# Optimization experiments

Measured on AMD Instinct MI355X. Metric: run time of the kernel, lower is better.

Reference implementation:

```python
import jax, jax.numpy as jnp
import numpy as np

V, D, L, H, HD, S = 50257, 768, 8, 6, 128, 2048
BS = 128          # flex-attention BLOCK_SIZE
EOS = 50256       # document separator token
EPS = 1.1920929e-07  # torch F.rms_norm default eps (f32 machine eps)
ATTN_SCALE = 0.12


def rms(x):
    return x * jax.lax.rsqrt(jnp.mean(jnp.square(x), axis=-1, keepdims=True) + EPS)


def rope_tables(seq_len, hd):
    # modded-nanogpt rotary: hd//4 geometric freqs + hd//4 zero freqs, applied to half-split dims
    freqs = (1.0 / 1024.0) ** jnp.linspace(0.0, 1.0, hd // 4)
    freqs = jnp.concatenate([freqs, jnp.zeros(hd // 4, dtype=jnp.float32)])
    theta = jnp.arange(seq_len, dtype=jnp.float32)[:, None] * freqs[None, :]  # [S, hd//2]
    return jnp.cos(theta), jnp.sin(theta)


def rope(x, cos, sin):  # x: [B,S,H,hd]
    x1, x2 = jnp.split(x, 2, axis=-1)
    c = cos[None, :, None, :]
    s = sin[None, :, None, :]
    return jnp.concatenate([x1 * c + x2 * s, -x1 * s + x2 * c], axis=-1)


def build_token_mask(input_seq, w):
    # Reproduces BlockMask.from_kv_blocks semantics: per query-row keep the w-1 most
    # recent FULL blocks and min(n_partial, max(w - n_full, 1)) most recent PARTIAL
    # blocks; mask_mod (document-causal) applies inside partial blocks only.
    NB = S // BS
    docs = jnp.cumsum((input_seq == EOS).astype(jnp.int32))
    bi = jnp.arange(NB)
    dr = docs.reshape(NB, BS)
    dl, dh = dr[:, 0], dr[:, -1]
    m_any = (bi[:, None] >= bi[None, :]) & (dl[:, None] <= dh[None, :]) & (dh[:, None] >= dl[None, :])
    m_all = (bi[:, None] > bi[None, :]) & (dl[:, None] == dh[None, :]) & (dh[:, None] == dl[None, :])
    part = m_any & ~m_all
    nf = m_all.sum(-1)

    def keep_most_recent(m, kcount):  # keep kcount True entries with largest kv index
        r = jnp.cumsum(m[:, ::-1].astype(jnp.int32), axis=-1)[:, ::-1]
        return m & (r <= kcount[:, None])

    kf = keep_most_recent(m_all, jnp.minimum(nf, w - 1))
    kp = keep_most_recent(part, jnp.minimum(part.sum(-1), jnp.maximum(w - nf, 1)))
    tf = jnp.repeat(jnp.repeat(kf, BS, 0), BS, 1)   # [S,S]
    tp = jnp.repeat(jnp.repeat(kp, BS, 0), BS, 1)
    q = jnp.arange(S)
    tok = (q[:, None] >= q[None, :]) & (docs[:, None] == docs[None, :])
    return tf | (tp & tok)


def _forward(input_seq, sliding_window_num_blocks, target_seq, embed, ve_embeds,
             qkv_w, attn_proj_w, mlp_fc_w, mlp_proj_w, scalars):
    cos, sin = rope_tables(S, HD)
    long_m = build_token_mask(input_seq, sliding_window_num_blocks)
    short_m = build_token_mask(input_seq, sliding_window_num_blocks // 2)
    cycle = [long_m, short_m, short_m, short_m]
    masks = (cycle * ((L + 3) // 4))[:L - 1] + [long_m]

    ve_tok = ve_embeds[:, input_seq, :]  # [3,S,D]
    ve = [ve_tok[0], ve_tok[1], ve_tok[2]] + [None] * (L - 6) + [ve_tok[0], ve_tok[1], ve_tok[2]]

    skip_w = scalars[:L]
    lambdas = scalars[L:3 * L].reshape(L, 2)
    sa_lambdas = scalars[3 * L:5 * L].reshape(L, 2)

    stride = max(1, L // 4)
    skip_map = {}
    for m in range(3):
        i = L - 3 + m
        j = i - stride * (m + 1)
        if 0 <= j < i < L:
            skip_map[i] = j

    x = x0 = rms(embed[input_seq])[None]  # [1,S,D]
    skips = []
    for i in range(L):
        if i in skip_map:
            x = x + skip_w[skip_map[i]] * skips[skip_map[i]]
        lam, sal = lambdas[i], sa_lambdas[i]
        # Block: residual mix with x0, attn, mlp (modded-nanogpt style)
        x = lam[0] * x + lam[1] * x0
        xa = rms(x)
        qkv = (xa @ qkv_w[i].T).reshape(1, S, 3 * H, HD)
        q, k, v = jnp.split(qkv, 3, axis=2)
        q = rope(rms(q), cos, sin)
        k = rope(rms(k), cos, sin)
        if ve[i] is not None:
            v = sal[0] * v + sal[1] * ve[i].reshape(1, S, H, HD)
        else:
            v = sal[0] * v
        scores = jnp.einsum('bqhd,bkhd->bhqk', q, k) * ATTN_SCALE
        scores = jnp.where(masks[i][None, None], scores, -jnp.inf)
        y = jnp.einsum('bhqk,bkhd->bqhd', jax.nn.softmax(scores, axis=-1), v)
        x = x + y.reshape(1, S, H * HD) @ attn_proj_w[i].T
        h = jnp.square(jax.nn.relu(rms(x) @ mlp_fc_w[i].T))
        x = x + h @ mlp_proj_w[i].T
        skips.append(x)

    x = rms(x)
    logits = (x[0].astype(jnp.bfloat16) @ embed.T.astype(jnp.bfloat16)).astype(jnp.float32)
    cap = 15.0 * logits * jax.lax.rsqrt(jnp.square(logits) + 225.0)  # softcap
    lsm = jax.nn.log_softmax(cap, axis=-1)
    return -jnp.mean(lsm[jnp.arange(S), target_seq])


def setup_inputs() -> dict:
    key = jax.random.key(0)
    ks = jax.random.split(key, 9)
    input_seq = jax.random.randint(ks[0], (S,), 0, V)
    input_seq = input_seq.at[jnp.arange(0, S, 512)].set(EOS)  # inject doc boundaries
    target_seq = jax.random.randint(ks[1], (S,), 0, V)
    embed = jax.random.normal(ks[2], (V, D), jnp.float32)
    ve_embeds = jax.random.normal(ks[3], (3, V, D), jnp.float32)
    sd = 1.0 / np.sqrt(D)
    qkv_w = jax.random.normal(ks[4], (L, 3 * H * HD, D), jnp.float32) * sd
    attn_proj_w = jax.random.normal(ks[5], (L, D, H * HD), jnp.float32) * (1.0 / np.sqrt(H * HD))
    mlp_fc_w = jax.random.normal(ks[6], (L, 4 * D, D), jnp.float32) * sd
    mlp_proj_w = jax.random.normal(ks[7], (L, D, 4 * D), jnp.float32) * (1.0 / np.sqrt(4 * D))
    scalars = jnp.concatenate([
        jnp.ones(L), jnp.tile(jnp.array([1.0, 0.0]), L), jnp.tile(jnp.array([0.5, 0.5]), L)
    ]).astype(jnp.float32) + 0.02 * jax.random.normal(ks[8], (5 * L,), jnp.float32)
    return {"input_seq": input_seq, "sliding_window_num_blocks": 8, "target_seq": target_seq,
            "embed": embed, "ve_embeds": ve_embeds, "qkv_w": qkv_w, "attn_proj_w": attn_proj_w,
            "mlp_fc_w": mlp_fc_w, "mlp_proj_w": mlp_proj_w, "scalars": scalars}


def reference(input_seq, sliding_window_num_blocks, target_seq, embed, ve_embeds,
              qkv_w, attn_proj_w, mlp_fc_w, mlp_proj_w, scalars):
    return _forward(input_seq, sliding_window_num_blocks, target_seq, embed, ve_embeds,
                    qkv_w, attn_proj_w, mlp_fc_w, mlp_proj_w, scalars)
```

## Files before the change

### kernel.cpp

```cpp
#include <hip/hip_runtime.h>
#include <hip/hip_bf16.h>
#include <math.h>

#define NSEQ 2048
#define NDIM 768
#define NLAY 8
#define NHEAD 6
#define NHD 128
#define NVOC 50257
#define NBLK 16
#define BLKSZ 128
#define EOS_TOK 50256
#define EPSF 1.1920929e-07f
#define ASCALE 0.12f
#define NVT 393

using bf16x8 = __attribute__((ext_vector_type(8))) __bf16;
using bf16x4 = __attribute__((ext_vector_type(4))) __bf16;
using f32x4  = __attribute__((ext_vector_type(4))) float;

__device__ __forceinline__ __bf16 tobf(float x) {
  __hip_bfloat16 h = __float2bfloat16(x);
  return *reinterpret_cast<__bf16*>(&h);
}

__global__ __launch_bounds__(256) void cvt_bf16_kernel(const float* __restrict__ in, __bf16* __restrict__ out,
                                                       long n) {
  long i = ((long)blockIdx.x * blockDim.x + threadIdx.x) * 4;
  long stride = (long)gridDim.x * blockDim.x * 4;
  for (; i < n; i += stride) {
    float4 v = *(const float4*)(in + i);
    bf16x4 o;
    o[0] = tobf(v.x); o[1] = tobf(v.y); o[2] = tobf(v.z); o[3] = tobf(v.w);
    *(bf16x4*)(out + i) = o;
  }
}

__global__ __launch_bounds__(1024) void prep_kernel(const int* __restrict__ seq, const int* __restrict__ wptr,
                                                    int* __restrict__ docs, int* __restrict__ catL,
                                                    int* __restrict__ catS) {
  __shared__ int f[NSEQ];
  __shared__ int g[NSEQ];
  int tid = threadIdx.x;
  for (int i = tid; i < NSEQ; i += 1024) f[i] = (seq[i] == EOS_TOK) ? 1 : 0;
  __syncthreads();
  int* a = f; int* b = g;
  for (int off = 1; off < NSEQ; off <<= 1) {
    for (int i = tid; i < NSEQ; i += 1024) {
      int v = a[i];
      if (i >= off) v += a[i - off];
      b[i] = v;
    }
    __syncthreads();
    int* t = a; a = b; b = t;
  }
  for (int i = tid; i < NSEQ; i += 1024) docs[i] = a[i];
  __syncthreads();
  if (tid == 0) {
    int dl[NBLK], dh[NBLK];
    for (int bi = 0; bi < NBLK; ++bi) { dl[bi] = a[bi * BLKSZ]; dh[bi] = a[bi * BLKSZ + BLKSZ - 1]; }
    int W = *wptr;
    for (int pass = 0; pass < 2; ++pass) {
      int w = (pass == 0) ? W : (W / 2);
      int* cat = (pass == 0) ? catL : catS;
      for (int i = 0; i < NBLK; ++i) {
        int allr[NBLK], partr[NBLK];
        int nf = 0, np = 0;
        for (int j = 0; j < NBLK; ++j) {
          int any_ = (i >= j) && (dl[i] <= dh[j]) && (dh[i] >= dl[j]);
          int all_ = (i > j) && (dl[i] == dh[j]) && (dh[i] == dl[j]);
          allr[j] = all_; partr[j] = any_ && !all_;
          nf += all_; np += partr[j];
        }
        int kcf = min(nf, w - 1);
        int kcp = min(np, max(w - nf, 1));
        int cf = 0, cp = 0;
        for (int j = NBLK - 1; j >= 0; --j) {
          int cv = 0;
          if (allr[j]) { cf++; if (cf <= kcf) cv = 2; }
          if (partr[j]) { cp++; if (cp <= kcp) cv = 1; }
          cat[i * NBLK + j] = cv;
        }
      }
    }
  }
}

__global__ __launch_bounds__(256) void embed_rms_kernel(const int* __restrict__ seq, const float* __restrict__ embed,
                                                        float* __restrict__ x, float* __restrict__ x0) {
  int s = blockIdx.x;
  int tid = threadIdx.x;
  const float* row = embed + (size_t)seq[s] * NDIM;
  float v0 = row[tid], v1 = row[tid + 256], v2 = row[tid + 512];
  float ss = v0 * v0 + v1 * v1 + v2 * v2;
  __shared__ float red[256];
  red[tid] = ss; __syncthreads();
  for (int o = 128; o > 0; o >>= 1) { if (tid < o) red[tid] += red[tid + o]; __syncthreads(); }
  float sc = rsqrtf(red[0] / (float)NDIM + EPSF);
  size_t base = (size_t)s * NDIM;
  float o0 = v0 * sc, o1 = v1 * sc, o2 = v2 * sc;
  x[base + tid] = o0; x[base + tid + 256] = o1; x[base + tid + 512] = o2;
  x0[base + tid] = o0; x0[base + tid + 256] = o1; x0[base + tid + 512] = o2;
}

__global__ __launch_bounds__(256) void rmsbf_kernel(const float* __restrict__ x, __bf16* __restrict__ xb) {
  int s = blockIdx.x;
  int tid = threadIdx.x;
  size_t base = (size_t)s * NDIM;
  float v0 = x[base + tid], v1 = x[base + tid + 256], v2 = x[base + tid + 512];
  float ss = v0 * v0 + v1 * v1 + v2 * v2;
  __shared__ float red[256];
  red[tid] = ss; __syncthreads();
  for (int o = 128; o > 0; o >>= 1) { if (tid < o) red[tid] += red[tid + o]; __syncthreads(); }
  float sc = rsqrtf(red[0] / (float)NDIM + EPSF);
  xb[base + tid] = tobf(v0 * sc); xb[base + tid + 256] = tobf(v1 * sc); xb[base + tid + 512] = tobf(v2 * sc);
}

__global__ __launch_bounds__(256) void mixrms_kernel(float* __restrict__ x, const float* __restrict__ x0,
                                                     const float* __restrict__ skip, const float* __restrict__ scal,
                                                     int li, int sj, __bf16* __restrict__ xb) {
  float lam0 = scal[NLAY + 2 * li], lam1 = scal[NLAY + 2 * li + 1];
  float sw = (sj >= 0) ? scal[sj] : 0.f;
  int s = blockIdx.x;
  int tid = threadIdx.x;
  size_t base = (size_t)s * NDIM;
  float xv[3], ov[3], nv[3];
  xv[0] = x[base + tid]; xv[1] = x[base + tid + 256]; xv[2] = x[base + tid + 512];
  ov[0] = x0[base + tid]; ov[1] = x0[base + tid + 256]; ov[2] = x0[base + tid + 512];
  if (skip) {
    nv[0] = lam0 * (xv[0] + sw * skip[base + tid])       + lam1 * ov[0];
    nv[1] = lam0 * (xv[1] + sw * skip[base + tid + 256]) + lam1 * ov[1];
    nv[2] = lam0 * (xv[2] + sw * skip[base + tid + 512]) + lam1 * ov[2];
  } else {
    nv[0] = lam0 * xv[0] + lam1 * ov[0];
    nv[1] = lam0 * xv[1] + lam1 * ov[1];
    nv[2] = lam0 * xv[2] + lam1 * ov[2];
  }
  x[base + tid] = nv[0]; x[base + tid + 256] = nv[1]; x[base + tid + 512] = nv[2];
  float ss = nv[0] * nv[0] + nv[1] * nv[1] + nv[2] * nv[2];
  __shared__ float red[256];
  red[tid] = ss; __syncthreads();
  for (int o = 128; o > 0; o >>= 1) { if (tid < o) red[tid] += red[tid + o]; __syncthreads(); }
  float sc = rsqrtf(red[0] / (float)NDIM + EPSF);
  xb[base + tid] = tobf(nv[0] * sc); xb[base + tid + 256] = tobf(nv[1] * sc); xb[base + tid + 512] = tobf(nv[2] * sc);
}

template <int MODE>
__global__ __launch_bounds__(256) void gemm_mfma(const __bf16* __restrict__ A, const __bf16* __restrict__ B,
                                                 float* __restrict__ Cf, __bf16* __restrict__ Cb,
                                                 int N, int K) {
  __shared__ __bf16 As[2][128 * 32];
  __shared__ __bf16 Bs[2][128 * 32];
  int bm = blockIdx.x * 128, bn = blockIdx.y * 128;
  int tid = threadIdx.x;
  int w = tid >> 6, l = tid & 63;
  int wm = (w >> 1) * 64, wn = (w & 1) * 64;
  int c = l & 15, g = l >> 4;

  auto stage = [&](int buf, int k0) {
#pragma unroll
    for (int i = 0; i < 2; ++i) {
      int L = (w * 2 + i) * 64 + l;
      int row = L >> 2, gc = L & 3;
      const __bf16* srcA = A + (size_t)(bm + row) * K + k0 + gc * 8;
      const __bf16* srcB = B + (size_t)(bn + row) * K + k0 + gc * 8;
      __builtin_amdgcn_global_load_lds(
          (const __attribute__((address_space(1))) void*)srcA,
          (__attribute__((address_space(3))) void*)&As[buf][(w * 2 + i) * 512], 16, 0, 0);
      __builtin_amdgcn_global_load_lds(
          (const __attribute__((address_space(1))) void*)srcB,
          (__attribute__((address_space(3))) void*)&Bs[buf][(w * 2 + i) * 512], 16, 0, 0);
    }
  };

  f32x4 acc[4][4] = {};
  stage(0, 0);
  __syncthreads();
  int nk = K >> 5;
  for (int kk = 0; kk < nk; ++kk) {
    int buf = kk & 1;
    if (kk + 1 < nk) stage(buf ^ 1, (kk + 1) * 32);
    bf16x8 af[4], bfr[4];
#pragma unroll
    for (int i = 0; i < 4; ++i) af[i] = *(const bf16x8*)&As[buf][(wm + i * 16 + c) * 32 + g * 8];
#pragma unroll
    for (int j = 0; j < 4; ++j) bfr[j] = *(const bf16x8*)&Bs[buf][(wn + j * 16 + c) * 32 + g * 8];
#pragma unroll
    for (int i = 0; i < 4; ++i)
#pragma unroll
      for (int j = 0; j < 4; ++j)
        acc[i][j] = __builtin_amdgcn_mfma_f32_16x16x32_bf16(af[i], bfr[j], acc[i][j], 0, 0, 0);
    __syncthreads();
  }
#pragma unroll
  for (int i = 0; i < 4; ++i)
#pragma unroll
    for (int j = 0; j < 4; ++j)
#pragma unroll
      for (int rr = 0; rr < 4; ++rr) {
        int row = bm + wm + i * 16 + g * 4 + rr;
        int col = bn + wn + j * 16 + c;
        size_t ci = (size_t)row * N + col;
        float z = acc[i][j][rr];
        if (MODE == 0) Cf[ci] = z;
        else if (MODE == 1) Cf[ci] += z;
        else { float r = fmaxf(z, 0.f); Cb[ci] = tobf(r * r); }
      }
}

template <int MODE>
__global__ __launch_bounds__(256) void gemm_mfma64(const __bf16* __restrict__ A, const __bf16* __restrict__ B,
                                                   float* __restrict__ Cf, __bf16* __restrict__ Cb,
                                                   int N, int K) {
  __shared__ __bf16 As[2][64 * 32];
  __shared__ __bf16 Bs[2][64 * 32];
  int bm = blockIdx.x * 64, bn = blockIdx.y * 64;
  int tid = threadIdx.x;
  int w = tid >> 6, l = tid & 63;
  int wm = (w >> 1) * 32, wn = (w & 1) * 32;
  int c = l & 15, g = l >> 4;

  auto stage = [&](int buf, int k0) {
    int L = w * 64 + l;
    int row = L >> 2, gc = L & 3;
    const __bf16* srcA = A + (size_t)(bm + row) * K + k0 + gc * 8;
    const __bf16* srcB = B + (size_t)(bn + row) * K + k0 + gc * 8;
    __builtin_amdgcn_global_load_lds(
        (const __attribute__((address_space(1))) void*)srcA,
        (__attribute__((address_space(3))) void*)&As[buf][w * 512], 16, 0, 0);
    __builtin_amdgcn_global_load_lds(
        (const __attribute__((address_space(1))) void*)srcB,
        (__attribute__((address_space(3))) void*)&Bs[buf][w * 512], 16, 0, 0);
  };

  f32x4 acc[2][2] = {};
  stage(0, 0);
  __syncthreads();
  int nk = K >> 5;
  for (int kk = 0; kk < nk; ++kk) {
    int buf = kk & 1;
    if (kk + 1 < nk) stage(buf ^ 1, (kk + 1) * 32);
    bf16x8 af[2], bfr[2];
#pragma unroll
    for (int i = 0; i < 2; ++i) af[i] = *(const bf16x8*)&As[buf][(wm + i * 16 + c) * 32 + g * 8];
#pragma unroll
    for (int j = 0; j < 2; ++j) bfr[j] = *(const bf16x8*)&Bs[buf][(wn + j * 16 + c) * 32 + g * 8];
#pragma unroll
    for (int i = 0; i < 2; ++i)
#pragma unroll
      for (int j = 0; j < 2; ++j)
        acc[i][j] = __builtin_amdgcn_mfma_f32_16x16x32_bf16(af[i], bfr[j], acc[i][j], 0, 0, 0);
    __syncthreads();
  }
#pragma unroll
  for (int i = 0; i < 2; ++i)
#pragma unroll
    for (int j = 0; j < 2; ++j)
#pragma unroll
      for (int rr = 0; rr < 4; ++rr) {
        int row = bm + wm + i * 16 + g * 4 + rr;
        int col = bn + wn + j * 16 + c;
        size_t ci = (size_t)row * N + col;
        float z = acc[i][j][rr];
        if (MODE == 0) Cf[ci] = z;
        else if (MODE == 1) Cf[ci] += z;
        else { float r = fmaxf(z, 0.f); Cb[ci] = tobf(r * r); }
      }
}

__global__ __launch_bounds__(256) void qkv_post_kernel(const float* __restrict__ qkv, const float* __restrict__ vemb,
                                                       const int* __restrict__ seq, const float* __restrict__ scal,
                                                       int li, int ve_idx,
                                                       __bf16* __restrict__ qo, __bf16* __restrict__ ko,
                                                       __bf16* __restrict__ vo) {
  int p = blockIdx.x * 4 + (threadIdx.x >> 6);
  int l = threadIdx.x & 63;
  int h = p >> 11;
  int s = p & (NSEQ - 1);
  float sal0 = scal[3 * NLAY + 2 * li], sal1 = scal[3 * NLAY + 2 * li + 1];
  float fr = (l < 32) ? powf(1.0f / 1024.0f, (float)l * (1.0f / 31.0f)) : 0.f;
  float th = (float)s * fr;
  float cth = cosf(th), sth = sinf(th);
  size_t rb = (size_t)s * (3 * NHEAD * NHD) + h * NHD;
  float q0 = qkv[rb + l],                 q1 = qkv[rb + l + 64];
  float k0 = qkv[rb + NHEAD * NHD + l],   k1 = qkv[rb + NHEAD * NHD + l + 64];
  float v0 = qkv[rb + 2 * NHEAD * NHD + l], v1 = qkv[rb + 2 * NHEAD * NHD + l + 64];
  float ssq = q0 * q0 + q1 * q1;
  float ssk = k0 * k0 + k1 * k1;
#pragma unroll
  for (int o = 1; o < 64; o <<= 1) {
    ssq += __shfl_xor(ssq, o, 64);
    ssk += __shfl_xor(ssk, o, 64);
  }
  float scq = rsqrtf(ssq / (float)NHD + EPSF);
  float sck = rsqrtf(ssk / (float)NHD + EPSF);
  float qn0 = q0 * scq, qn1 = q1 * scq;
  float kn0 = k0 * sck, kn1 = k1 * sck;
  float oq0 = qn0 * cth + qn1 * sth, oq1 = -qn0 * sth + qn1 * cth;
  float ok0 = kn0 * cth + kn1 * sth, ok1 = -kn0 * sth + kn1 * cth;
  float ov0 = sal0 * v0, ov1 = sal0 * v1;
  if (ve_idx >= 0) {
    const float* ver = vemb + ((size_t)ve_idx * NVOC + seq[s]) * NDIM + h * NHD;
    ov0 += sal1 * ver[l];
    ov1 += sal1 * ver[l + 64];
  }
  size_t oo = ((size_t)h * NSEQ + s) * NHD;
  qo[oo + l] = tobf(oq0); qo[oo + l + 64] = tobf(oq1);
  ko[oo + l] = tobf(ok0); ko[oo + l + 64] = tobf(ok1);
  vo[oo + l] = tobf(ov0); vo[oo + l + 64] = tobf(ov1);
}

__global__ __launch_bounds__(256) void vtrans_kernel(const __bf16* __restrict__ v, __bf16* __restrict__ vt) {
  int st = blockIdx.x * 64, dt = blockIdx.y * 64, h = blockIdx.z;
  __shared__ __bf16 t[64][65];
  int tid = threadIdx.x;
  for (int e = tid; e < 4096; e += 256) {
    int s = e >> 6, d = e & 63;
    t[s][d] = v[((size_t)h * NSEQ + st + s) * NHD + dt + d];
  }
  __syncthreads();
  for (int e = tid; e < 512; e += 256) {
    int d = e >> 3, s0 = (e & 7) * 8;
    bf16x8 ov;
#pragma unroll
    for (int i = 0; i < 8; ++i) ov[i] = t[s0 + i][d];
    *(bf16x8*)(vt + ((size_t)h * NHD + dt + d) * NSEQ + st + s0) = ov;
  }
}

__global__ __launch_bounds__(128) void attn_mfma_kernel(const __bf16* __restrict__ qb, const __bf16* __restrict__ kb,
                                                        const __bf16* __restrict__ vt, const int* __restrict__ cat,
                                                        const int* __restrict__ docs, __bf16* __restrict__ y) {
  int qb32 = (int)gridDim.x - 1 - (int)blockIdx.x;
  int h = blockIdx.y;
  int tid = threadIdx.x;
  int wq = tid >> 6;
  int l = tid & 63;
  int c = l & 15, g = l >> 4;
  int q0 = qb32 * 32 + wq * 16;
  int qB = qb32 >> 2;

  __shared__ __bf16 Ks[2][32 * 128];
  __shared__ __bf16 Vts[2][32 * 128];
  __shared__ __bf16 Ps[2][16 * 32];
  __shared__ int kvs[64];
  __shared__ int kvc[64];
  __shared__ int nact_s;

  if (tid == 0) {
    int n = 0;
    for (int kv = 0; kv <= qb32; ++kv) {
      int cc = cat[qB * NBLK + (kv >> 2)];
      if (cc) { kvs[n] = kv; kvc[n] = cc; ++n; }
    }
    nact_s = n;
  }

  bf16x8 qf[4];
#pragma unroll
  for (int ks = 0; ks < 4; ++ks)
    qf[ks] = *(const bf16x8*)(qb + ((size_t)h * NSEQ + q0 + c) * NHD + ks * 32 + g * 8);

  int qd[4];
#pragma unroll
  for (int rr = 0; rr < 4; ++rr) qd[rr] = docs[q0 + g * 4 + rr];

  float m[4], lden[4];
#pragma unroll
  for (int rr = 0; rr < 4; ++rr) { m[rr] = -INFINITY; lden[rr] = 0.f; }
  f32x4 oacc[8] = {};

  __syncthreads();
  int nact = nact_s;

  auto stage = [&](int kv, int bufi) {
#pragma unroll
    for (int i = 0; i < 4; ++i) {
      int L = (wq * 4 + i) * 64 + l;
      int krow = L >> 4, gl = L & 15;
      int gs = gl ^ (krow & 7);
      const __bf16* srcK = kb + ((size_t)h * NSEQ + kv * 32 + krow) * NHD + gs * 8;
      __builtin_amdgcn_global_load_lds(
          (const __attribute__((address_space(1))) void*)srcK,
          (__attribute__((address_space(3))) void*)&Ks[bufi][(wq * 4 + i) * 512], 16, 0, 0);
      int drow = L >> 2, gk = L & 3;
      const __bf16* srcV = vt + ((size_t)h * NHD + drow) * NSEQ + kv * 32 + gk * 8;
      __builtin_amdgcn_global_load_lds(
          (const __attribute__((address_space(1))) void*)srcV,
          (__attribute__((address_space(3))) void*)&Vts[bufi][(wq * 4 + i) * 512], 16, 0, 0);
    }
  };

  stage(kvs[0], 0);
  __syncthreads();

  for (int it = 0; it < nact; ++it) {
    int buf = it & 1;
    if (it + 1 < nact) stage(kvs[it + 1], buf ^ 1);
    int kv = kvs[it], cc = kvc[it];
    int k0 = kv * 32;

    f32x4 sacc[2] = {};
#pragma unroll
    for (int ks = 0; ks < 4; ++ks) {
#pragma unroll
      for (int j = 0; j < 2; ++j) {
        int row = j * 16 + c;
        int gi = (ks * 4 + g) ^ (row & 7);
        bf16x8 kf = *(const bf16x8*)&Ks[buf][row * 128 + gi * 8];
        sacc[j] = __builtin_amdgcn_mfma_f32_16x16x32_bf16(qf[ks], kf, sacc[j], 0, 0, 0);
      }
    }
    float sc[2][4];
    float bmax[4] = {-INFINITY, -INFINITY, -INFINITY, -INFINITY};
#pragma unroll
    for (int j = 0; j < 2; ++j) {
      int key = k0 + j * 16 + c;
      int kdj = docs[key];
#pragma unroll
      for (int rr = 0; rr < 4; ++rr) {
        int qrow = q0 + g * 4 + rr;
        bool ok = (cc == 2) || ((key <= qrow) && (kdj == qd[rr]));
        float z = ok ? sacc[j][rr] * ASCALE : -INFINITY;
        sc[j][rr] = z;
        bmax[rr] = fmaxf(bmax[rr], z);
      }
    }
#pragma unroll
    for (int rr = 0; rr < 4; ++rr) {
      bmax[rr] = fmaxf(bmax[rr], __shfl_xor(bmax[rr], 1, 64));
      bmax[rr] = fmaxf(bmax[rr], __shfl_xor(bmax[rr], 2, 64));
      bmax[rr] = fmaxf(bmax[rr], __shfl_xor(bmax[rr], 4, 64));
      bmax[rr] = fmaxf(bmax[rr], __shfl_xor(bmax[rr], 8, 64));
    }
    float corr[4], psum[4];
#pragma unroll
    for (int rr = 0; rr < 4; ++rr) {
      float mnew = fmaxf(m[rr], bmax[rr]);
      float msafe = (mnew == -INFINITY) ? 0.f : mnew;
      corr[rr] = __expf(m[rr] - msafe);
      float p0 = __expf(sc[0][rr] - msafe);
      float p1 = __expf(sc[1][rr] - msafe);
      sc[0][rr] = p0; sc[1][rr] = p1;
      psum[rr] = p0 + p1;
      m[rr] = mnew;
    }
#pragma unroll
    for (int rr = 0; rr < 4; ++rr) {
      psum[rr] += __shfl_xor(psum[rr], 1, 64);
      psum[rr] += __shfl_xor(psum[rr], 2, 64);
      psum[rr] += __shfl_xor(psum[rr], 4, 64);
      psum[rr] += __shfl_xor(psum[rr], 8, 64);
      lden[rr] = lden[rr] * corr[rr] + psum[rr];
    }
#pragma unroll
    for (int nt = 0; nt < 8; ++nt)
#pragma unroll
      for (int rr = 0; rr < 4; ++rr) oacc[nt][rr] *= corr[rr];
#pragma unroll
    for (int j = 0; j < 2; ++j)
#pragma unroll
      for (int rr = 0; rr < 4; ++rr)
        Ps[wq][(g * 4 + rr) * 32 + j * 16 + c] = tobf(sc[j][rr]);
    asm volatile("s_waitcnt lgkmcnt(0)" ::: "memory");
    bf16x8 pf = *(const bf16x8*)&Ps[wq][c * 32 + g * 8];
#pragma unroll
    for (int nt = 0; nt < 8; ++nt) {
      bf16x8 vf = *(const bf16x8*)&Vts[buf][(nt * 16 + c) * 32 + g * 8];
      oacc[nt] = __builtin_amdgcn_mfma_f32_16x16x32_bf16(pf, vf, oacc[nt], 0, 0, 0);
    }
    __syncthreads();
  }
  float inv[4];
#pragma unroll
  for (int rr = 0; rr < 4; ++rr) inv[rr] = (lden[rr] > 0.f) ? 1.f / lden[rr] : 0.f;
#pragma unroll
  for (int nt = 0; nt < 8; ++nt)
#pragma unroll
    for (int rr = 0; rr < 4; ++rr) {
      int qrow = q0 + g * 4 + rr;
      y[(size_t)qrow * NDIM + h * NHD + nt * 16 + c] = tobf(oacc[nt][rr] * inv[rr]);
    }
}

__global__ __launch_bounds__(256) void logits_gemm_kernel(const __bf16* __restrict__ xbf,
                                                          const __bf16* __restrict__ embed_bf,
                                                          const int* __restrict__ target,
                                                          float* __restrict__ part_m, float* __restrict__ part_l,
                                                          float* __restrict__ tcap) {
  __shared__ __bf16 As[2][128 * 32];
  __shared__ __bf16 Bs[2][128 * 32];
  __shared__ float rm2[2][128];
  __shared__ float rs2[2][128];
  int bm = blockIdx.x * 128;
  int vt = blockIdx.y;
  int bn = vt * 128;
  int tid = threadIdx.x;
  int w = tid >> 6, l = tid & 63;
  int wm = (w >> 1) * 64, wn = (w & 1) * 64;
  int c = l & 15, g = l >> 4;

  auto stage = [&](int buf, int k0) {
#pragma unroll
    for (int i = 0; i < 2; ++i) {
      int L = (w * 2 + i) * 64 + l;
      int row = L >> 2, gc = L & 3;
      int vrow = bn + row;
      if (vrow >= NVOC) vrow = NVOC - 1;
      const __bf16* srcA = xbf + (size_t)(bm + row) * NDIM + k0 + gc * 8;
      const __bf16* srcB = embed_bf + (size_t)vrow * NDIM + k0 + gc * 8;
      __builtin_amdgcn_global_load_lds(
          (const __attribute__((address_space(1))) void*)srcA,
          (__attribute__((address_space(3))) void*)&As[buf][(w * 2 + i) * 512], 16, 0, 0);
      __builtin_amdgcn_global_load_lds(
          (const __attribute__((address_space(1))) void*)srcB,
          (__attribute__((address_space(3))) void*)&Bs[buf][(w * 2 + i) * 512], 16, 0, 0);
    }
  };

  f32x4 acc[4][4] = {};
  stage(0, 0);
  __syncthreads();
  const int nk = NDIM / 32;
  for (int kk = 0; kk < nk; ++kk) {
    int buf = kk & 1;
    if (kk + 1 < nk) stage(buf ^ 1, (kk + 1) * 32);
    bf16x8 af[4], bfr[4];
#pragma unroll
    for (int i = 0; i < 4; ++i) af[i] = *(const bf16x8*)&As[buf][(wm + i * 16 + c) * 32 + g * 8];
#pragma unroll
    for (int j = 0; j < 4; ++j) bfr[j] = *(const bf16x8*)&Bs[buf][(wn + j * 16 + c) * 32 + g * 8];
#pragma unroll
    for (int i = 0; i < 4; ++i)
#pragma unroll
      for (int j = 0; j < 4; ++j)
        acc[i][j] = __builtin_amdgcn_mfma_f32_16x16x32_bf16(af[i], bfr[j], acc[i][j], 0, 0, 0);
    __syncthreads();
  }

#pragma unroll
  for (int i = 0; i < 4; ++i) {
#pragma unroll
    for (int rr = 0; rr < 4; ++rr) {
      int rowl = wm + i * 16 + g * 4 + rr;
      int tg = target[bm + rowl];
      float tmax = -INFINITY;
#pragma unroll
      for (int j = 0; j < 4; ++j) {
        int vv = bn + wn + j * 16 + c;
        bool okv = vv < NVOC;
        float z = acc[i][j][rr];
        float cp = okv ? 15.f * z * rsqrtf(z * z + 225.f) : -INFINITY;
        tmax = fmaxf(tmax, cp);
        if (okv && vv == tg) tcap[bm + rowl] = cp;
      }
      tmax = fmaxf(tmax, __shfl_xor(tmax, 1, 64));
      tmax = fmaxf(tmax, __shfl_xor(tmax, 2, 64));
      tmax = fmaxf(tmax, __shfl_xor(tmax, 4, 64));
      tmax = fmaxf(tmax, __shfl_xor(tmax, 8, 64));
      float ts = 0.f;
#pragma unroll
      for (int j = 0; j < 4; ++j) {
        int vv = bn + wn + j * 16 + c;
        bool okv = vv < NVOC;
        float z = acc[i][j][rr];
        float cp = 15.f * z * rsqrtf(z * z + 225.f);
        ts += okv ? __expf(cp - tmax) : 0.f;
      }
      ts += __shfl_xor(ts, 1, 64);
      ts += __shfl_xor(ts, 2, 64);
      ts += __shfl_xor(ts, 4, 64);
      ts += __shfl_xor(ts, 8, 64);
      if (c == 0) { rm2[w & 1][rowl] = tmax; rs2[w & 1][rowl] = ts; }
    }
  }
  __syncthreads();
  if (tid < 128) {
    float m0 = rm2[0][tid], m1 = rm2[1][tid];
    float s0 = rs2[0][tid], s1 = rs2[1][tid];
    float mn = fmaxf(m0, m1);
    float ls = s0 * __expf(m0 - mn) + s1 * __expf(m1 - mn);
    part_m[(size_t)vt * NSEQ + bm + tid] = mn;
    part_l[(size_t)vt * NSEQ + bm + tid] = ls;
  }
}

__global__ __launch_bounds__(256) void lossrow_kernel(const float* __restrict__ part_m, const float* __restrict__ part_l,
                                                      const float* __restrict__ tcap, float* __restrict__ lr) {
  int row = blockIdx.x * 256 + threadIdx.x;
  float M = -INFINITY;
  for (int cc = 0; cc < NVT; ++cc) M = fmaxf(M, part_m[(size_t)cc * NSEQ + row]);
  float L = 0.f;
  for (int cc = 0; cc < NVT; ++cc) L += part_l[(size_t)cc * NSEQ + row] * __expf(part_m[(size_t)cc * NSEQ + row] - M);
  lr[row] = (M + logf(L)) - tcap[row];
}

__global__ __launch_bounds__(256) void loss2_kernel(const float* __restrict__ lr, float* __restrict__ out) {
  int tid = threadIdx.x;
  float sum = 0.f;
  for (int t = tid; t < NSEQ; t += 256) sum += lr[t];
  __shared__ float red[256];
  red[tid] = sum; __syncthreads();
  for (int o = 128; o > 0; o >>= 1) { if (tid < o) red[tid] += red[tid + o]; __syncthreads(); }
  if (tid == 0) out[0] = red[0] / (float)NSEQ;
}

extern "C" void kernel_launch(void* const* d_in, const int* in_sizes, int n_in,
                              void* d_out, int out_size, void* d_ws, size_t ws_size,
                              hipStream_t stream) {
  const int* seq   = (const int*)d_in[0];
  const int* wnb   = (const int*)d_in[1];
  const int* tgt   = (const int*)d_in[2];
  const float* embed = (const float*)d_in[3];
  const float* vemb  = (const float*)d_in[4];
  const float* qkvw  = (const float*)d_in[5];
  const float* aprj  = (const float*)d_in[6];
  const float* fcw   = (const float*)d_in[7];
  const float* prjw  = (const float*)d_in[8];
  const float* scal  = (const float*)d_in[9];
  float* out = (float*)d_out;

  char* w = (char*)d_ws;
  auto alloc = [&](size_t bytes) {
    char* p = w;
    w += (bytes + 255) & ~(size_t)255;
    return p;
  };
  int* docs = (int*)alloc(NSEQ * 4);
  int* catL = (int*)alloc(NBLK * NBLK * 4);
  int* catS = (int*)alloc(NBLK * NBLK * 4);
  float* x    = (float*)alloc((size_t)NSEQ * NDIM * 4);
  float* x0   = (float*)alloc((size_t)NSEQ * NDIM * 4);
  float* sk1  = (float*)alloc((size_t)NSEQ * NDIM * 4);
  float* sk2  = (float*)alloc((size_t)NSEQ * NDIM * 4);
  float* sk3  = (float*)alloc((size_t)NSEQ * NDIM * 4);
  float* qkvb = (float*)alloc((size_t)NSEQ * 3 * NHEAD * NHD * 4);
  __bf16* qbf2 = (__bf16*)alloc((size_t)NHEAD * NSEQ * NHD * 2);
  __bf16* kbf2 = (__bf16*)alloc((size_t)NHEAD * NSEQ * NHD * 2);
  __bf16* vbf2 = (__bf16*)alloc((size_t)NHEAD * NSEQ * NHD * 2);
  __bf16* vtbf = (__bf16*)alloc((size_t)NHEAD * NHD * NSEQ * 2);
  __bf16* xabf = (__bf16*)alloc((size_t)NSEQ * NDIM * 2);
  __bf16* ybf  = (__bf16*)alloc((size_t)NSEQ * NDIM * 2);
  __bf16* hbf  = (__bf16*)alloc((size_t)NSEQ * 4 * NDIM * 2);
  __bf16* xbf  = (__bf16*)alloc((size_t)NSEQ * NDIM * 2);
  float* pm   = (float*)alloc((size_t)NVT * NSEQ * 4);
  float* pl   = (float*)alloc((size_t)NVT * NSEQ * 4);
  float* tc   = (float*)alloc((size_t)NSEQ * 4);
  float* lrow = (float*)alloc((size_t)NSEQ * 4);
  __bf16* embbf = (__bf16*)alloc((size_t)NVOC * NDIM * 2);
  __bf16* qkvwbf = (__bf16*)alloc((size_t)NLAY * 3 * NHEAD * NHD * NDIM * 2);
  __bf16* aprjbf = (__bf16*)alloc((size_t)NLAY * NDIM * NDIM * 2);
  __bf16* fcwbf  = (__bf16*)alloc((size_t)NLAY * 4 * NDIM * NDIM * 2);
  __bf16* prjwbf = (__bf16*)alloc((size_t)NLAY * NDIM * 4 * NDIM * 2);
  float* skips[4] = {nullptr, sk1, sk2, sk3};

  cvt_bf16_kernel<<<2048, 256, 0, stream>>>(embed, embbf, (long)NVOC * NDIM);
  cvt_bf16_kernel<<<2048, 256, 0, stream>>>(qkvw, qkvwbf, (long)NLAY * 3 * NHEAD * NHD * NDIM);
  cvt_bf16_kernel<<<2048, 256, 0, stream>>>(aprj, aprjbf, (long)NLAY * NDIM * NDIM);
  cvt_bf16_kernel<<<2048, 256, 0, stream>>>(fcw, fcwbf, (long)NLAY * 4 * NDIM * NDIM);
  cvt_bf16_kernel<<<2048, 256, 0, stream>>>(prjw, prjwbf, (long)NLAY * NDIM * 4 * NDIM);

  prep_kernel<<<1, 1024, 0, stream>>>(seq, wnb, docs, catL, catS);
  embed_rms_kernel<<<NSEQ, 256, 0, stream>>>(seq, embed, x, x0);

  const int velist[NLAY]   = {0, 1, 2, -1, -1, 0, 1, 2};
  const int skipj[NLAY]    = {-1, -1, -1, -1, -1, 3, 2, 1};
  const int maskLong[NLAY] = {1, 0, 0, 0, 1, 0, 0, 1};

  for (int i = 0; i < NLAY; ++i) {
    mixrms_kernel<<<NSEQ, 256, 0, stream>>>(x, x0, skipj[i] >= 0 ? skips[skipj[i]] : nullptr, scal, i, skipj[i], xabf);
    gemm_mfma<0><<<dim3(NSEQ / 128, (3 * NHEAD * NHD) / 128), 256, 0, stream>>>(
        xabf, qkvwbf + (size_t)i * 3 * NHEAD * NHD * NDIM, qkvb, nullptr, 3 * NHEAD * NHD, NDIM);
    qkv_post_kernel<<<NHEAD * NSEQ / 4, 256, 0, stream>>>(qkvb, vemb, seq, scal, i, velist[i], qbf2, kbf2, vbf2);
    vtrans_kernel<<<dim3(NSEQ / 64, NHD / 64, NHEAD), 256, 0, stream>>>(vbf2, vtbf);
    attn_mfma_kernel<<<dim3(NSEQ / 32, NHEAD), 128, 0, stream>>>(qbf2, kbf2, vtbf, maskLong[i] ? catL : catS, docs, ybf);
    gemm_mfma64<1><<<dim3(NSEQ / 64, NDIM / 64), 256, 0, stream>>>(
        ybf, aprjbf + (size_t)i * NDIM * NDIM, x, nullptr, NDIM, NDIM);
    rmsbf_kernel<<<NSEQ, 256, 0, stream>>>(x, xabf);
    gemm_mfma<2><<<dim3(NSEQ / 128, (4 * NDIM) / 128), 256, 0, stream>>>(
        xabf, fcwbf + (size_t)i * 4 * NDIM * NDIM, nullptr, hbf, 4 * NDIM, NDIM);
    gemm_mfma64<1><<<dim3(NSEQ / 64, NDIM / 64), 256, 0, stream>>>(
        hbf, prjwbf + (size_t)i * NDIM * 4 * NDIM, x, nullptr, NDIM, 4 * NDIM);
    if (i >= 1 && i <= 3) {
      hipMemcpyAsync(skips[i], x, (size_t)NSEQ * NDIM * 4, hipMemcpyDeviceToDevice, stream);
    }
  }

  rmsbf_kernel<<<NSEQ, 256, 0, stream>>>(x, xbf);
  logits_gemm_kernel<<<dim3(NSEQ / 128, NVT), 256, 0, stream>>>(xbf, embbf, tgt, pm, pl, tc);
  lossrow_kernel<<<NSEQ / 256, 256, 0, stream>>>(pm, pl, tc, lrow);
  loss2_kernel<<<1, 256, 0, stream>>>(lrow, out);
}
```

Before: 2.015 ms.

## Split attention over KV range into four partitions with a merge kernel

```diff
diff --git a/kernel.cpp b/kernel.cpp
--- a/kernel.cpp
+++ b/kernel.cpp
@@ -14,6 +14,7 @@
 #define EPSF 1.1920929e-07f
 #define ASCALE 0.12f
 #define NVT 393
+#define NSPLIT 4
 
 using bf16x8 = __attribute__((ext_vector_type(8))) __bf16;
 using bf16x4 = __attribute__((ext_vector_type(4))) __bf16;
@@ -22,6 +23,10 @@
 __device__ __forceinline__ __bf16 tobf(float x) {
   __hip_bfloat16 h = __float2bfloat16(x);
   return *reinterpret_cast<__bf16*>(&h);
+}
+__device__ __forceinline__ float frombf(__bf16 x) {
+  __hip_bfloat16 h = *reinterpret_cast<__hip_bfloat16*>(&x);
+  return __bfloat162float(h);
 }
 
 __global__ __launch_bounds__(256) void cvt_bf16_kernel(const float* __restrict__ in, __bf16* __restrict__ out,
@@ -330,9 +335,12 @@
 
 __global__ __launch_bounds__(128) void attn_mfma_kernel(const __bf16* __restrict__ qb, const __bf16* __restrict__ kb,
                                                         const __bf16* __restrict__ vt, const int* __restrict__ cat,
-                                                        const int* __restrict__ docs, __bf16* __restrict__ y) {
+                                                        const int* __restrict__ docs,
+                                                        __bf16* __restrict__ po, float* __restrict__ pma,
+                                                        float* __restrict__ pla) {
   int qb32 = (int)gridDim.x - 1 - (int)blockIdx.x;
   int h = blockIdx.y;
+  int sp = blockIdx.z;
   int tid = threadIdx.x;
   int wq = tid >> 6;
   int l = tid & 63;
@@ -347,9 +355,12 @@
   __shared__ int kvc[64];
   __shared__ int nact_s;
 
+  int ntile = qb32 + 1;
+  int lo = (sp * ntile) / NSPLIT;
+  int hi = ((sp + 1) * ntile) / NSPLIT;
   if (tid == 0) {
     int n = 0;
-    for (int kv = 0; kv <= qb32; ++kv) {
+    for (int kv = lo; kv < hi; ++kv) {
       int cc = cat[qB * NBLK + (kv >> 2)];
       if (cc) { kvs[n] = kv; kvc[n] = cc; ++n; }
     }
@@ -391,96 +402,130 @@
     }
   };
 
-  stage(kvs[0], 0);
-  __syncthreads();
-
-  for (int it = 0; it < nact; ++it) {
-    int buf = it & 1;
-    if (it + 1 < nact) stage(kvs[it + 1], buf ^ 1);
-    int kv = kvs[it], cc = kvc[it];
-    int k0 = kv * 32;
-
-    f32x4 sacc[2] = {};
-#pragma unroll
-    for (int ks = 0; ks < 4; ++ks) {
+  if (nact > 0) {
+    stage(kvs[0], 0);
+    __syncthreads();
+
+    for (int it = 0; it < nact; ++it) {
+      int buf = it & 1;
+      if (it + 1 < nact) stage(kvs[it + 1], buf ^ 1);
+      int kv = kvs[it], cc = kvc[it];
+      int k0 = kv * 32;
+
+      f32x4 sacc[2] = {};
+#pragma unroll
+      for (int ks = 0; ks < 4; ++ks) {
+#pragma unroll
+        for (int j = 0; j < 2; ++j) {
+          int row = j * 16 + c;
+          int gi = (ks * 4 + g) ^ (row & 7);
+          bf16x8 kf = *(const bf16x8*)&Ks[buf][row * 128 + gi * 8];
+          sacc[j] = __builtin_amdgcn_mfma_f32_16x16x32_bf16(qf[ks], kf, sacc[j], 0, 0, 0);
+        }
+      }
+      float sc[2][4];
+      float bmax[4] = {-INFINITY, -INFINITY, -INFINITY, -INFINITY};
 #pragma unroll
       for (int j = 0; j < 2; ++j) {
-        int row = j * 16 + c;
-        int gi = (ks * 4 + g) ^ (row & 7);
-        bf16x8 kf = *(const bf16x8*)&Ks[buf][row * 128 + gi * 8];
-        sacc[j] = __builtin_amdgcn_mfma_f32_16x16x32_bf16(qf[ks], kf, sacc[j], 0, 0, 0);
-      }
-    }
-    float sc[2][4];
-    float bmax[4] = {-INFINITY, -INFINITY, -INFINITY, -INFINITY};
-#pragma unroll
-    for (int j = 0; j < 2; ++j) {
-      int key = k0 + j * 16 + c;
-      int kdj = docs[key];
+        int key = k0 + j * 16 + c;
+        int kdj = docs[key];
+#pragma unroll
+        for (int rr = 0; rr < 4; ++rr) {
+          int qrow = q0 + g * 4 + rr;
+          bool ok = (cc == 2) || ((key <= qrow) && (kdj == qd[rr]));
+          float z = ok ? sacc[j][rr] * ASCALE : -INFINITY;
+          sc[j][rr] = z;
+          bmax[rr] = fmaxf(bmax[rr], z);
+        }
+      }
 #pragma unroll
       for (int rr = 0; rr < 4; ++rr) {
-        int qrow = q0 + g * 4 + rr;
-        bool ok = (cc == 2) || ((key <= qrow) && (kdj == qd[rr]));
-        float z = ok ? sacc[j][rr] * ASCALE : -INFINITY;
-        sc[j][rr] = z;
-        bmax[rr] = fmaxf(bmax[rr], z);
-      }
-    }
-#pragma unroll
-    for (int rr = 0; rr < 4; ++rr) {
-      bmax[rr] = fmaxf(bmax[rr], __shfl_xor(bmax[rr], 1, 64));
-      bmax[rr] = fmaxf(bmax[rr], __shfl_xor(bmax[rr], 2, 64));
-      bmax[rr] = fmaxf(bmax[rr], __shfl_xor(bmax[rr], 4, 64));
-      bmax[rr] = fmaxf(bmax[rr], __shfl_xor(bmax[rr], 8, 64));
-    }
-    float corr[4], psum[4];
-#pragma unroll
-    for (int rr = 0; rr < 4; ++rr) {
-      float mnew = fmaxf(m[rr], bmax[rr]);
-      float msafe = (mnew == -INFINITY) ? 0.f : mnew;
-      corr[rr] = __expf(m[rr] - msafe);
-      float p0 = __expf(sc[0][rr] - msafe);
-      float p1 = __expf(sc[1][rr] - msafe);
-      sc[0][rr] = p0; sc[1][rr] = p1;
-      psum[rr] = p0 + p1;
-      m[rr] = mnew;
-    }
-#pragma unroll
-    for (int rr = 0; rr < 4; ++rr) {
-      psum[rr] += __shfl_xor(psum[rr], 1, 64);
-      psum[rr] += __shfl_xor(psum[rr], 2, 64);
-      psum[rr] += __shfl_xor(psum[rr], 4, 64);
-      psum[rr] += __shfl_xor(psum[rr], 8, 64);
-      lden[rr] = lden[rr] * corr[rr] + psum[rr];
-    }
-#pragma unroll
-    for (int nt = 0; nt < 8; ++nt)
-#pragma unroll
-      for (int rr = 0; rr < 4; ++rr) oacc[nt][rr] *= corr[rr];
-#pragma unroll
-    for (int j = 0; j < 2; ++j)
-#pragma unroll
-      for (int rr = 0; rr < 4; ++rr)
-        Ps[wq][(g * 4 + rr) * 32 + j * 16 + c] = tobf(sc[j][rr]);
-    asm volatile("s_waitcnt lgkmcnt(0)" ::: "memory");
-    bf16x8 pf = *(const bf16x8*)&Ps[wq][c * 32 + g * 8];
-#pragma unroll
-    for (int nt = 0; nt < 8; ++nt) {
-      bf16x8 vf = *(const bf16x8*)&Vts[buf][(nt * 16 + c) * 32 + g * 8];
-      oacc[nt] = __builtin_amdgcn_mfma_f32_16x16x32_bf16(pf, vf, oacc[nt], 0, 0, 0);
-    }
-    __syncthreads();
-  }
-  float inv[4];
-#pragma unroll
-  for (int rr = 0; rr < 4; ++rr) inv[rr] = (lden[rr] > 0.f) ? 1.f / lden[rr] : 0.f;
+        bmax[rr] = fmaxf(bmax[rr], __shfl_xor(bmax[rr], 1, 64));
+        bmax[rr] = fmaxf(bmax[rr], __shfl_xor(bmax[rr], 2, 64));
+        bmax[rr] = fmaxf(bmax[rr], __shfl_xor(bmax[rr], 4, 64));
+        bmax[rr] = fmaxf(bmax[rr], __shfl_xor(bmax[rr], 8, 64));
+      }
+      float corr[4], psum[4];
+#pragma unroll
+      for (int rr = 0; rr < 4; ++rr) {
+        float mnew = fmaxf(m[rr], bmax[rr]);
+        float msafe = (mnew == -INFINITY) ? 0.f : mnew;
+        corr[rr] = __expf(m[rr] - msafe);
+        float p0 = __expf(sc[0][rr] - msafe);
+        float p1 = __expf(sc[1][rr] - msafe);
+        sc[0][rr] = p0; sc[1][rr] = p1;
+        psum[rr] = p0 + p1;
+        m[rr] = mnew;
+      }
+#pragma unroll
+      for (int rr = 0; rr < 4; ++rr) {
+        psum[rr] += __shfl_xor(psum[rr], 1, 64);
+        psum[rr] += __shfl_xor(psum[rr], 2, 64);
+        psum[rr] += __shfl_xor(psum[rr], 4, 64);
+        psum[rr] += __shfl_xor(psum[rr], 8, 64);
+        lden[rr] = lden[rr] * corr[rr] + psum[rr];
+      }
+#pragma unroll
+      for (int nt = 0; nt < 8; ++nt)
+#pragma unroll
+        for (int rr = 0; rr < 4; ++rr) oacc[nt][rr] *= corr[rr];
+#pragma unroll
+      for (int j = 0; j < 2; ++j)
+#pragma unroll
+        for (int rr = 0; rr < 4; ++rr)
+          Ps[wq][(g * 4 + rr) * 32 + j * 16 + c] = tobf(sc[j][rr]);
+      asm volatile("s_waitcnt lgkmcnt(0)" ::: "memory");
+      bf16x8 pf = *(const bf16x8*)&Ps[wq][c * 32 + g * 8];
+#pragma unroll
+      for (int nt = 0; nt < 8; ++nt) {
+        bf16x8 vf = *(const bf16x8*)&Vts[buf][(nt * 16 + c) * 32 + g * 8];
+        oacc[nt] = __builtin_amdgcn_mfma_f32_16x16x32_bf16(pf, vf, oacc[nt], 0, 0, 0);
+      }
+      __syncthreads();
+    }
+  }
+
+  size_t pb = ((size_t)(sp * NHEAD + h)) * NSEQ;
 #pragma unroll
   for (int nt = 0; nt < 8; ++nt)
 #pragma unroll
     for (int rr = 0; rr < 4; ++rr) {
       int qrow = q0 + g * 4 + rr;
-      y[(size_t)qrow * NDIM + h * NHD + nt * 16 + c] = tobf(oacc[nt][rr] * inv[rr]);
-    }
+      po[(pb + qrow) * NHD + nt * 16 + c] = tobf(oacc[nt][rr]);
+    }
+  if (c == 0) {
+#pragma unroll
+    for (int rr = 0; rr < 4; ++rr) {
+      int qrow = q0 + g * 4 + rr;
+      pma[pb + qrow] = m[rr];
+      pla[pb + qrow] = lden[rr];
+    }
+  }
+}
+
+__global__ __launch_bounds__(128) void attn_merge_kernel(const __bf16* __restrict__ po,
+                                                         const float* __restrict__ pma,
+                                                         const float* __restrict__ pla,
+                                                         __bf16* __restrict__ y) {
+  int row = blockIdx.x;
+  int d = threadIdx.x;
+  for (int h = 0; h < NHEAD; ++h) {
+    float M = -INFINITY;
+#pragma unroll
+    for (int sp = 0; sp < NSPLIT; ++sp) M = fmaxf(M, pma[(size_t)(sp * NHEAD + h) * NSEQ + row]);
+    float L = 0.f, acc = 0.f;
+#pragma unroll
+    for (int sp = 0; sp < NSPLIT; ++sp) {
+      size_t pb = (size_t)(sp * NHEAD + h) * NSEQ + row;
+      float mc = pma[pb];
+      if (mc > -INFINITY) {
+        float wgt = __expf(mc - M);
+        L += pla[pb] * wgt;
+        acc += frombf(po[pb * NHD + d]) * wgt;
+      }
+    }
+    y[(size_t)row * NDIM + h * NHD + d] = tobf(acc / L);
+  }
 }
 
 __global__ __launch_bounds__(256) void logits_gemm_kernel(const __bf16* __restrict__ xbf,
@@ -654,6 +699,10 @@
   __bf16* prjwbf = (__bf16*)alloc((size_t)NLAY * NDIM * 4 * NDIM * 2);
   float* skips[4] = {nullptr, sk1, sk2, sk3};
 
+  __bf16* po  = (__bf16*)qkvb;
+  float*  pma = (float*)((char*)qkvb + (size_t)NSPLIT * NHEAD * NSEQ * NHD * 2);
+  float*  pla = pma + (size_t)NSPLIT * NHEAD * NSEQ;
+
   cvt_bf16_kernel<<<2048, 256, 0, stream>>>(embed, embbf, (long)NVOC * NDIM);
   cvt_bf16_kernel<<<2048, 256, 0, stream>>>(qkvw, qkvwbf, (long)NLAY * 3 * NHEAD * NHD * NDIM);
   cvt_bf16_kernel<<<2048, 256, 0, stream>>>(aprj, aprjbf, (long)NLAY * NDIM * NDIM);
@@ -673,7 +722,9 @@
         xabf, qkvwbf + (size_t)i * 3 * NHEAD * NHD * NDIM, qkvb, nullptr, 3 * NHEAD * NHD, NDIM);
     qkv_post_kernel<<<NHEAD * NSEQ / 4, 256, 0, stream>>>(qkvb, vemb, seq, scal, i, velist[i], qbf2, kbf2, vbf2);
     vtrans_kernel<<<dim3(NSEQ / 64, NHD / 64, NHEAD), 256, 0, stream>>>(vbf2, vtbf);
-    attn_mfma_kernel<<<dim3(NSEQ / 32, NHEAD), 128, 0, stream>>>(qbf2, kbf2, vtbf, maskLong[i] ? catL : catS, docs, ybf);
+    attn_mfma_kernel<<<dim3(NSEQ / 32, NHEAD, NSPLIT), 128, 0, stream>>>(
+        qbf2, kbf2, vtbf, maskLong[i] ? catL : catS, docs, po, pma, pla);
+    attn_merge_kernel<<<NSEQ, 128, 0, stream>>>(po, pma, pla, ybf);
     gemm_mfma64<1><<<dim3(NSEQ / 64, NDIM / 64), 256, 0, stream>>>(
         ybf, aprjbf + (size_t)i * NDIM * NDIM, x, nullptr, NDIM, NDIM);
     rmsbf_kernel<<<NSEQ, 256, 0, stream>>>(x, xabf);
```

Measured after the change: 2.169 ms. 7.7% more time.
